# Kernel tuning notes

Hardware: AMD Instinct MI355X
Metric: run time of the kernel (lower is better)

## Reference

```python
import jax, jax.numpy as jnp
import numpy as np

TEMPERATURE = 0.1
THRESHOLD = 0.2
EPS = 1e-12


def setup_inputs() -> dict:
    key = jax.random.key(0)
    k0, k1 = jax.random.split(key)
    f0 = jax.random.normal(k0, (1, 256, 80, 80), dtype=jnp.float32)
    f1 = jax.random.normal(k1, (1, 256, 80, 80), dtype=jnp.float32)
    return {"f0": f0, "f1": f1}


def reference(f0, f1):
    B, C, H0, W0 = f0.shape
    _, _, H1, W1 = f1.shape
    N0, N1 = H0 * W0, H1 * W1

    # (B, N, C), L2-normalized along C (matches F.normalize with eps clamp)
    f0_flat = f0.reshape(B, C, N0).transpose(0, 2, 1)
    f1_flat = f1.reshape(B, C, N1).transpose(0, 2, 1)
    f0n = f0_flat / jnp.maximum(jnp.linalg.norm(f0_flat, axis=-1, keepdims=True), EPS)
    f1n = f1_flat / jnp.maximum(jnp.linalg.norm(f1_flat, axis=-1, keepdims=True), EPS)

    # cosine similarity / temperature: (B, N0, N1)
    S = jnp.einsum('bnc,bmc->bnm', f0n, f1n) / TEMPERATURE
    # dual softmax
    P = jax.nn.softmax(S, axis=-1) * jax.nn.softmax(S, axis=-2)

    # mutual nearest-neighbor matching (B == 1 branch)
    conf = jnp.max(P[0], axis=-1)              # (N0,)
    indices0 = jnp.argmax(P[0], axis=-1)       # (N0,) row argmax
    indices1 = jnp.argmax(P[0], axis=-2)       # (N1,) column argmax
    ar0 = jnp.arange(N0)
    mutual = indices1[indices0] == ar0
    valid = mutual & (conf > THRESHOLD)        # (N0,) bool

    # fixed-shape (jit-friendly) match outputs: full grid, zeroed where invalid
    mkpts0 = jnp.stack([ar0 % W0, ar0 // W0], axis=1).astype(jnp.float32)
    mkpts1 = jnp.stack([indices0 % W1, indices0 // W1], axis=1).astype(jnp.float32)
    vf = valid[:, None].astype(jnp.float32)
    mkpts0 = mkpts0 * vf
    mkpts1 = mkpts1 * vf
    mconf = jnp.where(valid, conf, 0.0)

    return (P, mkpts0, mkpts1, mconf, valid)
```

## Files before the change

kernel.cpp:

```cpp
#include <hip/hip_runtime.h>

#define N0 6400
#define NC 256
#define WW 80

using half8   = __attribute__((ext_vector_type(8))) _Float16;
using floatx4 = __attribute__((ext_vector_type(4))) float;
#define GLOBAL_AS __attribute__((address_space(1)))
#define LDS_AS    __attribute__((address_space(3)))

__device__ __forceinline__ unsigned long long packvi(float v, int i) {
    return ((unsigned long long)__float_as_uint(v) << 32) | (unsigned int)i;
}

__global__ __launch_bounds__(256) void knorm(const float* __restrict__ f0,
                                             const float* __restrict__ f1,
                                             float* __restrict__ inv0,
                                             float* __restrict__ inv1) {
    int t = blockIdx.x * 256 + threadIdx.x;
    const float* src = (t < N0) ? f0 : f1;
    int n = (t < N0) ? t : (t - N0);
    float s = 0.f;
#pragma unroll 8
    for (int c = 0; c < NC; ++c) {
        float v = src[c * N0 + n];
        s += v * v;
    }
    float inv = 1.0f / fmaxf(sqrtf(s), 1e-12f);
    if (t < N0) inv0[n] = inv; else inv1[n] = inv;
}

__global__ __launch_bounds__(256) void ktrans(const float* __restrict__ f0,
                                              const float* __restrict__ f1,
                                              const float* __restrict__ inv0,
                                              const float* __restrict__ inv1,
                                              _Float16* __restrict__ A2,
                                              _Float16* __restrict__ B2) {
    __shared__ float tile[32][33];
    const float* src = blockIdx.z ? f1 : f0;
    const float* inv = blockIdx.z ? inv1 : inv0;
    _Float16* dst    = blockIdx.z ? B2 : A2;
    int t = threadIdx.x;
    int n0 = blockIdx.x * 32, c0 = blockIdx.y * 32;
    int tx = t & 31, ty = t >> 5;
#pragma unroll
    for (int u = 0; u < 4; ++u)
        tile[ty + u * 8][tx] = src[(c0 + ty + u * 8) * N0 + n0 + tx];
    __syncthreads();
    int row = t >> 3;
    int cg  = (t & 7) * 4;
    int n = n0 + row;
    float iv = inv[n];
    union { ushort4 u4; _Float16 h[4]; } pk;
#pragma unroll
    for (int u = 0; u < 4; ++u)
        pk.h[u] = (_Float16)(tile[cg + u][row] * iv);
    *(ushort4*)&dst[n * NC + c0 + cg] = pk.u4;
}

__device__ __forceinline__ void stage_panel(const _Float16* __restrict__ G,
                                            unsigned short* lds, int r0, int tid) {
    int rl = tid >> 3;
    int ch = ((tid & 7) ^ (rl & 7)) * 8;
#pragma unroll
    for (int kk = 0; kk < 4; ++kk)
#pragma unroll
        for (int g = 0; g < 4; ++g) {
            const _Float16* ga = G + (r0 + g * 32 + rl) * NC + kk * 64 + ch;
            __builtin_amdgcn_global_load_lds((const GLOBAL_AS unsigned int*)ga,
                (LDS_AS unsigned int*)&lds[kk * 8192 + g * 2048 + tid * 8], 16, 0, 0);
        }
}

__device__ __forceinline__ void tile_mfma(const unsigned short* ldsA,
                                          const unsigned short* ldsB,
                                          int lane, int wm, int wn,
                                          floatx4 acc[4][4]) {
    int q = lane >> 4;
#pragma unroll
    for (int s = 0; s < 8; ++s) {
        int c  = s * 4 + q;
        int kk = c >> 3, cq = c & 7;
        half8 af[4], bf[4];
#pragma unroll
        for (int mt = 0; mt < 4; ++mt) {
            int ra = wm * 64 + mt * 16 + (lane & 15);
            af[mt] = *(const half8*)&ldsA[kk * 8192 + ra * 64 + ((cq ^ (ra & 7)) * 8)];
            int rb = wn * 64 + mt * 16 + (lane & 15);
            bf[mt] = *(const half8*)&ldsB[kk * 8192 + rb * 64 + ((cq ^ (rb & 7)) * 8)];
        }
#pragma unroll
        for (int mt = 0; mt < 4; ++mt)
#pragma unroll
            for (int nt = 0; nt < 4; ++nt)
                acc[mt][nt] = __builtin_amdgcn_mfma_f32_16x16x32_f16(
                    af[mt], bf[nt], acc[mt][nt], 0, 0, 0);
    }
}

__global__ __launch_bounds__(256, 1) void kgemm1(const _Float16* __restrict__ A2,
                                                 const _Float16* __restrict__ B2,
                                                 float* __restrict__ rowsum,
                                                 float* __restrict__ colsum) {
    __shared__ __align__(16) unsigned short ldsA[32768], ldsB[32768];
    int tid = threadIdx.x, lane = tid & 63, wave = tid >> 6;
    int wm = wave & 1, wn = wave >> 1, q = lane >> 4;
    int i0 = blockIdx.x * 128, jp = blockIdx.y * 1280;

    stage_panel(A2, ldsA, i0, tid);
    float rsum[4][4] = {};

    for (int jt = 0; jt < 10; ++jt) {
        __syncthreads();
        stage_panel(B2, ldsB, jp + jt * 128, tid);
        __syncthreads();
        floatx4 acc[4][4] = {};
        tile_mfma(ldsA, ldsB, lane, wm, wn, acc);

        float csum[4] = {0.f, 0.f, 0.f, 0.f};
#pragma unroll
        for (int mt = 0; mt < 4; ++mt)
#pragma unroll
            for (int r = 0; r < 4; ++r) {
                float rv = 0.f;
#pragma unroll
                for (int nt = 0; nt < 4; ++nt) {
                    float e = __expf(10.0f * acc[mt][nt][r]);
                    rv += e; csum[nt] += e;
                }
                rsum[mt][r] += rv;
            }
#pragma unroll
        for (int nt = 0; nt < 4; ++nt) {
            csum[nt] += __shfl_xor(csum[nt], 16);
            csum[nt] += __shfl_xor(csum[nt], 32);
        }
        if (lane < 16)
#pragma unroll
            for (int nt = 0; nt < 4; ++nt)
                atomicAdd(&colsum[jp + jt * 128 + wn * 64 + nt * 16 + lane], csum[nt]);
    }
#pragma unroll
    for (int mt = 0; mt < 4; ++mt)
#pragma unroll
        for (int r = 0; r < 4; ++r) {
            float v = rsum[mt][r];
            v += __shfl_xor(v, 1);
            v += __shfl_xor(v, 2);
            v += __shfl_xor(v, 4);
            v += __shfl_xor(v, 8);
            if ((lane & 15) == 0)
                atomicAdd(&rowsum[i0 + wm * 64 + mt * 16 + q * 4 + r], v);
        }
}

__global__ __launch_bounds__(256, 1) void kgemm2(const _Float16* __restrict__ A2,
                                                 const _Float16* __restrict__ B2,
                                                 const float* __restrict__ rowsum,
                                                 const float* __restrict__ colsum,
                                                 float* __restrict__ P,
                                                 unsigned long long* __restrict__ rowbest,
                                                 unsigned long long* __restrict__ colbest) {
    __shared__ __align__(16) unsigned short ldsA[32768], ldsB[32768];
    int tid = threadIdx.x, lane = tid & 63, wave = tid >> 6;
    int wm = wave & 1, wn = wave >> 1, q = lane >> 4;
    int i0 = blockIdx.x * 128, jp = blockIdx.y * 1280;

    stage_panel(A2, ldsA, i0, tid);

    float ir[4][4];
#pragma unroll
    for (int mt = 0; mt < 4; ++mt) {
        float4 v4 = *(const float4*)&rowsum[i0 + wm * 64 + mt * 16 + q * 4];
        ir[mt][0] = 1.0f / v4.x; ir[mt][1] = 1.0f / v4.y;
        ir[mt][2] = 1.0f / v4.z; ir[mt][3] = 1.0f / v4.w;
    }

    unsigned long long rbv[4][4] = {};

    for (int jt = 0; jt < 10; ++jt) {
        __syncthreads();
        stage_panel(B2, ldsB, jp + jt * 128, tid);
        __syncthreads();
        floatx4 acc[4][4] = {};
        tile_mfma(ldsA, ldsB, lane, wm, wn, acc);

        int cb0 = jp + jt * 128 + wn * 64 + (lane & 15);
        float ic[4];
#pragma unroll
        for (int nt = 0; nt < 4; ++nt) ic[nt] = 1.0f / colsum[cb0 + nt * 16];

        unsigned long long colb[4] = {0ull, 0ull, 0ull, 0ull};
#pragma unroll
        for (int mt = 0; mt < 4; ++mt) {
            int rb0 = i0 + wm * 64 + mt * 16 + q * 4;
#pragma unroll
            for (int r = 0; r < 4; ++r) {
                int row = rb0 + r;
#pragma unroll
                for (int nt = 0; nt < 4; ++nt) {
                    float pv = __expf(20.0f * acc[mt][nt][r]) * ir[mt][r] * ic[nt];
                    P[row * N0 + cb0 + nt * 16] = pv;
                    unsigned long long pr = packvi(pv, cb0 + nt * 16);
                    if (pr > rbv[mt][r]) rbv[mt][r] = pr;
                    unsigned long long pc = packvi(pv, row);
                    if (pc > colb[nt]) colb[nt] = pc;
                }
            }
        }
#pragma unroll
        for (int nt = 0; nt < 4; ++nt) {
            unsigned long long o = __shfl_xor(colb[nt], 16);
            if (o > colb[nt]) colb[nt] = o;
            o = __shfl_xor(colb[nt], 32);
            if (o > colb[nt]) colb[nt] = o;
        }
        if (lane < 16)
#pragma unroll
            for (int nt = 0; nt < 4; ++nt)
                atomicMax(&colbest[cb0 + nt * 16], colb[nt]);
    }
#pragma unroll
    for (int mt = 0; mt < 4; ++mt)
#pragma unroll
        for (int r = 0; r < 4; ++r) {
            unsigned long long v = rbv[mt][r];
#pragma unroll
            for (int s = 1; s < 16; s <<= 1) {
                unsigned long long o = __shfl_xor(v, s);
                if (o > v) v = o;
            }
            if ((lane & 15) == 0)
                atomicMax(&rowbest[i0 + wm * 64 + mt * 16 + q * 4 + r], v);
        }
}

__global__ __launch_bounds__(256) void kmatch(const unsigned long long* __restrict__ rowbest,
                                              const unsigned long long* __restrict__ colbest,
                                              float* __restrict__ out) {
    int i = blockIdx.x * 256 + threadIdx.x;
    unsigned long long rb = rowbest[i];
    float conf = __uint_as_float((unsigned int)(rb >> 32));
    int jj = (int)(rb & 0xffffffffu);
    unsigned long long cb = colbest[jj];
    int i2 = (int)(cb & 0xffffffffu);
    bool valid = (i2 == i) && (conf > 0.2f);
    float vf = valid ? 1.0f : 0.0f;

    float* mk0   = out + 40960000;
    float* mk1   = out + 40972800;
    float* mconf = out + 40985600;
    float* vout  = out + 40992000;
    mk0[i * 2 + 0] = vf * (float)(i % WW);
    mk0[i * 2 + 1] = vf * (float)(i / WW);
    mk1[i * 2 + 0] = vf * (float)(jj % WW);
    mk1[i * 2 + 1] = vf * (float)(jj / WW);
    mconf[i] = valid ? conf : 0.0f;
    vout[i]  = vf;
}

extern "C" void kernel_launch(void* const* d_in, const int* in_sizes, int n_in,
                              void* d_out, int out_size, void* d_ws, size_t ws_size,
                              hipStream_t stream) {
    const float* f0 = (const float*)d_in[0];
    const float* f1 = (const float*)d_in[1];
    float* out = (float*)d_out;

    _Float16* A2 = (_Float16*)d_ws;
    _Float16* B2 = A2 + 6400 * 256;
    float* inv0   = (float*)(B2 + 6400 * 256);
    float* inv1   = inv0 + 6400;
    float* rowsum = inv1 + 6400;
    float* colsum = rowsum + 6400;
    unsigned long long* rowbest = (unsigned long long*)(colsum + 6400);
    unsigned long long* colbest = rowbest + 6400;

    hipMemsetAsync(rowsum, 0, 153600, stream);

    knorm<<<50, 256, 0, stream>>>(f0, f1, inv0, inv1);
    ktrans<<<dim3(200, 8, 2), 256, 0, stream>>>(f0, f1, inv0, inv1, A2, B2);
    kgemm1<<<dim3(50, 5), 256, 0, stream>>>(A2, B2, rowsum, colsum);
    kgemm2<<<dim3(50, 5), 256, 0, stream>>>(A2, B2, rowsum, colsum,
                                            out, rowbest, colbest);
    kmatch<<<25, 256, 0, stream>>>(rowbest, colbest, out);
}
```

Baseline: 275.1 us.

## Keep A fragments in registers and double-buffer B panels in LDS

Both GEMM kernels now load the A panel fragments into registers once, then reuse the whole 128KB LDS as two B-panel buffers. The next B panel is prefetched with global_load_lds while MFMAs run on the current one, leaving one barrier per iteration instead of two. The memset is also folded into knorm to remove a separate launch. The cost is heavy register pressure (128 VGPRs for A fragments plus accumulators), and the async LDS loads rely on the end-of-iteration barrier to be complete before the buffer is read.

Result: faster. 267.9 us (-2.6%).

```diff
diff --git a/kernel.cpp b/kernel.cpp
--- a/kernel.cpp
+++ b/kernel.cpp
@@ -16,8 +16,16 @@
 __global__ __launch_bounds__(256) void knorm(const float* __restrict__ f0,
                                              const float* __restrict__ f1,
                                              float* __restrict__ inv0,
-                                             float* __restrict__ inv1) {
+                                             float* __restrict__ inv1,
+                                             float* __restrict__ rowsum,
+                                             float* __restrict__ colsum,
+                                             unsigned long long* __restrict__ rowbest,
+                                             unsigned long long* __restrict__ colbest) {
     int t = blockIdx.x * 256 + threadIdx.x;
+    if (t < N0) {
+        rowsum[t] = 0.f; colsum[t] = 0.f;
+        rowbest[t] = 0ull; colbest[t] = 0ull;
+    }
     const float* src = (t < N0) ? f0 : f1;
     int n = (t < N0) ? t : (t - N0);
     float s = 0.f;
@@ -72,50 +80,54 @@
         }
 }
 
-__device__ __forceinline__ void tile_mfma(const unsigned short* ldsA,
-                                          const unsigned short* ldsB,
-                                          int lane, int wm, int wn,
-                                          floatx4 acc[4][4]) {
-    int q = lane >> 4;
-#pragma unroll
-    for (int s = 0; s < 8; ++s) {
-        int c  = s * 4 + q;
-        int kk = c >> 3, cq = c & 7;
-        half8 af[4], bf[4];
-#pragma unroll
-        for (int mt = 0; mt < 4; ++mt) {
-            int ra = wm * 64 + mt * 16 + (lane & 15);
-            af[mt] = *(const half8*)&ldsA[kk * 8192 + ra * 64 + ((cq ^ (ra & 7)) * 8)];
-            int rb = wn * 64 + mt * 16 + (lane & 15);
-            bf[mt] = *(const half8*)&ldsB[kk * 8192 + rb * 64 + ((cq ^ (rb & 7)) * 8)];
-        }
-#pragma unroll
-        for (int mt = 0; mt < 4; ++mt)
-#pragma unroll
-            for (int nt = 0; nt < 4; ++nt)
-                acc[mt][nt] = __builtin_amdgcn_mfma_f32_16x16x32_f16(
-                    af[mt], bf[nt], acc[mt][nt], 0, 0, 0);
-    }
-}
-
 __global__ __launch_bounds__(256, 1) void kgemm1(const _Float16* __restrict__ A2,
                                                  const _Float16* __restrict__ B2,
                                                  float* __restrict__ rowsum,
                                                  float* __restrict__ colsum) {
-    __shared__ __align__(16) unsigned short ldsA[32768], ldsB[32768];
+    __shared__ __align__(16) unsigned short lds[65536];
     int tid = threadIdx.x, lane = tid & 63, wave = tid >> 6;
     int wm = wave & 1, wn = wave >> 1, q = lane >> 4;
     int i0 = blockIdx.x * 128, jp = blockIdx.y * 1280;
 
-    stage_panel(A2, ldsA, i0, tid);
+    stage_panel(A2, lds, i0, tid);
+    stage_panel(B2, lds + 32768, jp, tid);
+    __syncthreads();
+
+    half8 af[4][8];
+#pragma unroll
+    for (int mt = 0; mt < 4; ++mt)
+#pragma unroll
+        for (int s = 0; s < 8; ++s) {
+            int c = s * 4 + q, kk = c >> 3, cq = c & 7;
+            int ra = wm * 64 + mt * 16 + (lane & 15);
+            af[mt][s] = *(const half8*)&lds[kk * 8192 + ra * 64 + ((cq ^ (ra & 7)) * 8)];
+        }
+    __syncthreads();
+
     float rsum[4][4] = {};
 
     for (int jt = 0; jt < 10; ++jt) {
-        __syncthreads();
-        stage_panel(B2, ldsB, jp + jt * 128, tid);
-        __syncthreads();
+        const unsigned short* cur = lds + ((jt & 1) ? 0 : 32768);
+        if (jt < 9)
+            stage_panel(B2, lds + ((jt & 1) ? 32768 : 0), jp + (jt + 1) * 128, tid);
+
         floatx4 acc[4][4] = {};
-        tile_mfma(ldsA, ldsB, lane, wm, wn, acc);
+#pragma unroll
+        for (int s = 0; s < 8; ++s) {
+            int c = s * 4 + q, kk = c >> 3, cq = c & 7;
+            half8 bf[4];
+#pragma unroll
+            for (int nt = 0; nt < 4; ++nt) {
+                int rb = wn * 64 + nt * 16 + (lane & 15);
+                bf[nt] = *(const half8*)&cur[kk * 8192 + rb * 64 + ((cq ^ (rb & 7)) * 8)];
+            }
+#pragma unroll
+            for (int mt = 0; mt < 4; ++mt)
+#pragma unroll
+                for (int nt = 0; nt < 4; ++nt)
+                    acc[mt][nt] = __builtin_amdgcn_mfma_f32_16x16x32_f16(
+                        af[mt][s], bf[nt], acc[mt][nt], 0, 0, 0);
+        }
 
         float csum[4] = {0.f, 0.f, 0.f, 0.f};
 #pragma unroll
@@ -139,6 +151,7 @@
 #pragma unroll
             for (int nt = 0; nt < 4; ++nt)
                 atomicAdd(&colsum[jp + jt * 128 + wn * 64 + nt * 16 + lane], csum[nt]);
+        __syncthreads();
     }
 #pragma unroll
     for (int mt = 0; mt < 4; ++mt)
@@ -161,12 +174,25 @@
                                                  float* __restrict__ P,
                                                  unsigned long long* __restrict__ rowbest,
                                                  unsigned long long* __restrict__ colbest) {
-    __shared__ __align__(16) unsigned short ldsA[32768], ldsB[32768];
+    __shared__ __align__(16) unsigned short lds[65536];
     int tid = threadIdx.x, lane = tid & 63, wave = tid >> 6;
     int wm = wave & 1, wn = wave >> 1, q = lane >> 4;
     int i0 = blockIdx.x * 128, jp = blockIdx.y * 1280;
 
-    stage_panel(A2, ldsA, i0, tid);
+    stage_panel(A2, lds, i0, tid);
+    stage_panel(B2, lds + 32768, jp, tid);
+    __syncthreads();
+
+    half8 af[4][8];
+#pragma unroll
+    for (int mt = 0; mt < 4; ++mt)
+#pragma unroll
+        for (int s = 0; s < 8; ++s) {
+            int c = s * 4 + q, kk = c >> 3, cq = c & 7;
+            int ra = wm * 64 + mt * 16 + (lane & 15);
+            af[mt][s] = *(const half8*)&lds[kk * 8192 + ra * 64 + ((cq ^ (ra & 7)) * 8)];
+        }
+    __syncthreads();
 
     float ir[4][4];
 #pragma unroll
@@ -179,11 +205,27 @@
     unsigned long long rbv[4][4] = {};
 
     for (int jt = 0; jt < 10; ++jt) {
-        __syncthreads();
-        stage_panel(B2, ldsB, jp + jt * 128, tid);
-        __syncthreads();
+        const unsigned short* cur = lds + ((jt & 1) ? 0 : 32768);
+        if (jt < 9)
+            stage_panel(B2, lds + ((jt & 1) ? 32768 : 0), jp + (jt + 1) * 128, tid);
+
         floatx4 acc[4][4] = {};
-        tile_mfma(ldsA, ldsB, lane, wm, wn, acc);
+#pragma unroll
+        for (int s = 0; s < 8; ++s) {
+            int c = s * 4 + q, kk = c >> 3, cq = c & 7;
+            half8 bf[4];
+#pragma unroll
+            for (int nt = 0; nt < 4; ++nt) {
+                int rb = wn * 64 + nt * 16 + (lane & 15);
+                bf[nt] = *(const half8*)&cur[kk * 8192 + rb * 64 + ((cq ^ (rb & 7)) * 8)];
+            }
+#pragma unroll
+            for (int mt = 0; mt < 4; ++mt)
+#pragma unroll
+                for (int nt = 0; nt < 4; ++nt)
+                    acc[mt][nt] = __builtin_amdgcn_mfma_f32_16x16x32_f16(
+                        af[mt][s], bf[nt], acc[mt][nt], 0, 0, 0);
+        }
 
         int cb0 = jp + jt * 128 + wn * 64 + (lane & 15);
         float ic[4];
@@ -219,6 +261,7 @@
 #pragma unroll
             for (int nt = 0; nt < 4; ++nt)
                 atomicMax(&colbest[cb0 + nt * 16], colb[nt]);
+        __syncthreads();
     }
 #pragma unroll
     for (int mt = 0; mt < 4; ++mt)
@@ -275,9 +318,8 @@
     unsigned long long* rowbest = (unsigned long long*)(colsum + 6400);
     unsigned long long* colbest = rowbest + 6400;
 
-    hipMemsetAsync(rowsum, 0, 153600, stream);
-
-    knorm<<<50, 256, 0, stream>>>(f0, f1, inv0, inv1);
+    knorm<<<50, 256, 0, stream>>>(f0, f1, inv0, inv1,
+                                  rowsum, colsum, rowbest, colbest);
     ktrans<<<dim3(200, 8, 2), 256, 0, stream>>>(f0, f1, inv0, inv1, A2, B2);
     kgemm1<<<dim3(50, 5), 256, 0, stream>>>(A2, B2, rowsum, colsum);
     kgemm2<<<dim3(50, 5), 256, 0, stream>>>(A2, B2, rowsum, colsum,
```

## Halve GEMM LDS footprint, keep A low-K in registers, double grid, fuse memset

Applied to the files above, without the earlier changes.

The GEMM kernels drop from 128KB to 64KB of LDS. The low half of the A panel's K dimension now lives in registers and the B panel is staged in two K-chunks, so two blocks can fit per CU. The column split is doubled to 10 so the grid grows from 250 to 500 blocks, which gives better CU coverage. The norm kernel is split across two channel halves for more parallelism, and it now zeroes the accumulators in place of the separate memset. The cost is extra barriers per tile, higher register pressure from holding the A fragments, and twice as many atomic updates.

Measured after the change: 280.9 us. +2.1%, slower.

```diff
diff --git a/kernel.cpp b/kernel.cpp
--- a/kernel.cpp
+++ b/kernel.cpp
@@ -15,30 +15,37 @@
 
 __global__ __launch_bounds__(256) void knorm(const float* __restrict__ f0,
                                              const float* __restrict__ f1,
-                                             float* __restrict__ inv0,
-                                             float* __restrict__ inv1) {
-    int t = blockIdx.x * 256 + threadIdx.x;
-    const float* src = (t < N0) ? f0 : f1;
-    int n = (t < N0) ? t : (t - N0);
+                                             float* __restrict__ snorm,
+                                             float* __restrict__ rowsum,
+                                             float* __restrict__ colsum,
+                                             unsigned long long* __restrict__ rowbest,
+                                             unsigned long long* __restrict__ colbest) {
+    int g = blockIdx.x * 256 + threadIdx.x;
+    if (g < N0) {
+        rowsum[g] = 0.f; colsum[g] = 0.f;
+        rowbest[g] = 0ull; colbest[g] = 0ull;
+    }
+    int h = (g >= 12800) ? 1 : 0;
+    int j = g - h * 12800;
+    const float* src = (j < N0) ? f0 : f1;
+    int n = (j < N0) ? j : (j - N0);
+    int c0 = h * 128;
     float s = 0.f;
 #pragma unroll 8
-    for (int c = 0; c < NC; ++c) {
-        float v = src[c * N0 + n];
+    for (int c = 0; c < 128; ++c) {
+        float v = src[(c0 + c) * N0 + n];
         s += v * v;
     }
-    float inv = 1.0f / fmaxf(sqrtf(s), 1e-12f);
-    if (t < N0) inv0[n] = inv; else inv1[n] = inv;
+    snorm[g] = s;
 }
 
 __global__ __launch_bounds__(256) void ktrans(const float* __restrict__ f0,
                                               const float* __restrict__ f1,
-                                              const float* __restrict__ inv0,
-                                              const float* __restrict__ inv1,
+                                              const float* __restrict__ snorm,
                                               _Float16* __restrict__ A2,
                                               _Float16* __restrict__ B2) {
     __shared__ float tile[32][33];
     const float* src = blockIdx.z ? f1 : f0;
-    const float* inv = blockIdx.z ? inv1 : inv0;
     _Float16* dst    = blockIdx.z ? B2 : A2;
     int t = threadIdx.x;
     int n0 = blockIdx.x * 32, c0 = blockIdx.y * 32;
@@ -50,7 +57,9 @@
     int row = t >> 3;
     int cg  = (t & 7) * 4;
     int n = n0 + row;
-    float iv = inv[n];
+    int j = (blockIdx.z ? N0 : 0) + n;
+    float s = snorm[j] + snorm[12800 + j];
+    float iv = 1.0f / fmaxf(sqrtf(s), 1e-12f);
     union { ushort4 u4; _Float16 h[4]; } pk;
 #pragma unroll
     for (int u = 0; u < 4; ++u)
@@ -58,36 +67,45 @@
     *(ushort4*)&dst[n * NC + c0 + cg] = pk.u4;
 }
 
-__device__ __forceinline__ void stage_panel(const _Float16* __restrict__ G,
-                                            unsigned short* lds, int r0, int tid) {
+__device__ __forceinline__ void stage_chunk(const _Float16* __restrict__ G,
+                                            unsigned short* lds, int r0, int kc,
+                                            int tid) {
     int rl = tid >> 3;
     int ch = ((tid & 7) ^ (rl & 7)) * 8;
 #pragma unroll
-    for (int kk = 0; kk < 4; ++kk)
+    for (int kk = 0; kk < 2; ++kk)
 #pragma unroll
         for (int g = 0; g < 4; ++g) {
-            const _Float16* ga = G + (r0 + g * 32 + rl) * NC + kk * 64 + ch;
+            const _Float16* ga = G + (r0 + g * 32 + rl) * NC + kc * 128 + kk * 64 + ch;
             __builtin_amdgcn_global_load_lds((const GLOBAL_AS unsigned int*)ga,
                 (LDS_AS unsigned int*)&lds[kk * 8192 + g * 2048 + tid * 8], 16, 0, 0);
         }
 }
 
-__device__ __forceinline__ void tile_mfma(const unsigned short* ldsA,
-                                          const unsigned short* ldsB,
-                                          int lane, int wm, int wn,
-                                          floatx4 acc[4][4]) {
+template<bool HI>
+__device__ __forceinline__ void compute_half(const unsigned short* bbuf,
+                                             const unsigned short* abufHi,
+                                             const half8 aflo[4][4],
+                                             int lane, int wm, int wn,
+                                             floatx4 acc[4][4]) {
     int q = lane >> 4;
 #pragma unroll
-    for (int s = 0; s < 8; ++s) {
-        int c  = s * 4 + q;
-        int kk = c >> 3, cq = c & 7;
+    for (int s = 0; s < 4; ++s) {
+        int c = s * 4 + q, kk = c >> 3, cq = c & 7;
         half8 af[4], bf[4];
 #pragma unroll
         for (int mt = 0; mt < 4; ++mt) {
-            int ra = wm * 64 + mt * 16 + (lane & 15);
-            af[mt] = *(const half8*)&ldsA[kk * 8192 + ra * 64 + ((cq ^ (ra & 7)) * 8)];
             int rb = wn * 64 + mt * 16 + (lane & 15);
-            bf[mt] = *(const half8*)&ldsB[kk * 8192 + rb * 64 + ((cq ^ (rb & 7)) * 8)];
+            bf[mt] = *(const half8*)&bbuf[kk * 8192 + rb * 64 + ((cq ^ (rb & 7)) * 8)];
+        }
+#pragma unroll
+        for (int mt = 0; mt < 4; ++mt) {
+            if (HI) {
+                int ra = wm * 64 + mt * 16 + (lane & 15);
+                af[mt] = *(const half8*)&abufHi[kk * 8192 + ra * 64 + ((cq ^ (ra & 7)) * 8)];
+            } else {
+                af[mt] = aflo[mt][s];
+            }
         }
 #pragma unroll
         for (int mt = 0; mt < 4; ++mt)
@@ -98,24 +116,42 @@
     }
 }
 
-__global__ __launch_bounds__(256, 1) void kgemm1(const _Float16* __restrict__ A2,
+__global__ __launch_bounds__(256, 2) void kgemm1(const _Float16* __restrict__ A2,
                                                  const _Float16* __restrict__ B2,
                                                  float* __restrict__ rowsum,
                                                  float* __restrict__ colsum) {
-    __shared__ __align__(16) unsigned short ldsA[32768], ldsB[32768];
+    __shared__ __align__(16) unsigned short lds[32768];
+    unsigned short* regA = lds;
+    unsigned short* regB = lds + 16384;
     int tid = threadIdx.x, lane = tid & 63, wave = tid >> 6;
     int wm = wave & 1, wn = wave >> 1, q = lane >> 4;
-    int i0 = blockIdx.x * 128, jp = blockIdx.y * 1280;
-
-    stage_panel(A2, ldsA, i0, tid);
+    int i0 = blockIdx.x * 128, jp = blockIdx.y * 640;
+
+    stage_chunk(A2, regB, i0, 0, tid);
+    stage_chunk(A2, regA, i0, 1, tid);
+    __syncthreads();
+    half8 aflo[4][4];
+#pragma unroll
+    for (int mt = 0; mt < 4; ++mt)
+#pragma unroll
+        for (int s = 0; s < 4; ++s) {
+            int c = s * 4 + q, kk = c >> 3, cq = c & 7;
+            int ra = wm * 64 + mt * 16 + (lane & 15);
+            aflo[mt][s] = *(const half8*)&regB[kk * 8192 + ra * 64 + ((cq ^ (ra & 7)) * 8)];
+        }
+    __syncthreads();
+
     float rsum[4][4] = {};
 
-    for (int jt = 0; jt < 10; ++jt) {
-        __syncthreads();
-        stage_panel(B2, ldsB, jp + jt * 128, tid);
+    for (int jt = 0; jt < 5; ++jt) {
+        stage_chunk(B2, regB, jp + jt * 128, 0, tid);
         __syncthreads();
         floatx4 acc[4][4] = {};
-        tile_mfma(ldsA, ldsB, lane, wm, wn, acc);
+        compute_half<false>(regB, regA, aflo, lane, wm, wn, acc);
+        __syncthreads();
+        stage_chunk(B2, regB, jp + jt * 128, 1, tid);
+        __syncthreads();
+        compute_half<true>(regB, regA, aflo, lane, wm, wn, acc);
 
         float csum[4] = {0.f, 0.f, 0.f, 0.f};
 #pragma unroll
@@ -139,6 +175,7 @@
 #pragma unroll
             for (int nt = 0; nt < 4; ++nt)
                 atomicAdd(&colsum[jp + jt * 128 + wn * 64 + nt * 16 + lane], csum[nt]);
+        __syncthreads();
     }
 #pragma unroll
     for (int mt = 0; mt < 4; ++mt)
@@ -154,19 +191,33 @@
         }
 }
 
-__global__ __launch_bounds__(256, 1) void kgemm2(const _Float16* __restrict__ A2,
+__global__ __launch_bounds__(256, 2) void kgemm2(const _Float16* __restrict__ A2,
                                                  const _Float16* __restrict__ B2,
                                                  const float* __restrict__ rowsum,
                                                  const float* __restrict__ colsum,
                                                  float* __restrict__ P,
                                                  unsigned long long* __restrict__ rowbest,
                                                  unsigned long long* __restrict__ colbest) {
-    __shared__ __align__(16) unsigned short ldsA[32768], ldsB[32768];
+    __shared__ __align__(16) unsigned short lds[32768];
+    unsigned short* regA = lds;
+    unsigned short* regB = lds + 16384;
     int tid = threadIdx.x, lane = tid & 63, wave = tid >> 6;
     int wm = wave & 1, wn = wave >> 1, q = lane >> 4;
-    int i0 = blockIdx.x * 128, jp = blockIdx.y * 1280;
-
-    stage_panel(A2, ldsA, i0, tid);
+    int i0 = blockIdx.x * 128, jp = blockIdx.y * 640;
+
+    stage_chunk(A2, regB, i0, 0, tid);
+    stage_chunk(A2, regA, i0, 1, tid);
+    __syncthreads();
+    half8 aflo[4][4];
+#pragma unroll
+    for (int mt = 0; mt < 4; ++mt)
+#pragma unroll
+        for (int s = 0; s < 4; ++s) {
+            int c = s * 4 + q, kk = c >> 3, cq = c & 7;
+            int ra = wm * 64 + mt * 16 + (lane & 15);
+            aflo[mt][s] = *(const half8*)&regB[kk * 8192 + ra * 64 + ((cq ^ (ra & 7)) * 8)];
+        }
+    __syncthreads();
 
     float ir[4][4];
 #pragma unroll
@@ -178,12 +229,15 @@
 
     unsigned long long rbv[4][4] = {};
 
-    for (int jt = 0; jt < 10; ++jt) {
-        __syncthreads();
-        stage_panel(B2, ldsB, jp + jt * 128, tid);
+    for (int jt = 0; jt < 5; ++jt) {
+        stage_chunk(B2, regB, jp + jt * 128, 0, tid);
         __syncthreads();
         floatx4 acc[4][4] = {};
-        tile_mfma(ldsA, ldsB, lane, wm, wn, acc);
+        compute_half<false>(regB, regA, aflo, lane, wm, wn, acc);
+        __syncthreads();
+        stage_chunk(B2, regB, jp + jt * 128, 1, tid);
+        __syncthreads();
+        compute_half<true>(regB, regA, aflo, lane, wm, wn, acc);
 
         int cb0 = jp + jt * 128 + wn * 64 + (lane & 15);
         float ic[4];
@@ -219,6 +273,7 @@
 #pragma unroll
             for (int nt = 0; nt < 4; ++nt)
                 atomicMax(&colbest[cb0 + nt * 16], colb[nt]);
+        __syncthreads();
     }
 #pragma unroll
     for (int mt = 0; mt < 4; ++mt)
@@ -268,19 +323,17 @@
 
     _Float16* A2 = (_Float16*)d_ws;
     _Float16* B2 = A2 + 6400 * 256;
-    float* inv0   = (float*)(B2 + 6400 * 256);
-    float* inv1   = inv0 + 6400;
-    float* rowsum = inv1 + 6400;
+    float* snorm  = (float*)(B2 + 6400 * 256);
+    float* rowsum = snorm + 25600;
     float* colsum = rowsum + 6400;
     unsigned long long* rowbest = (unsigned long long*)(colsum + 6400);
     unsigned long long* colbest = rowbest + 6400;
 
-    hipMemsetAsync(rowsum, 0, 153600, stream);
-
-    knorm<<<50, 256, 0, stream>>>(f0, f1, inv0, inv1);
-    ktrans<<<dim3(200, 8, 2), 256, 0, stream>>>(f0, f1, inv0, inv1, A2, B2);
-    kgemm1<<<dim3(50, 5), 256, 0, stream>>>(A2, B2, rowsum, colsum);
-    kgemm2<<<dim3(50, 5), 256, 0, stream>>>(A2, B2, rowsum, colsum,
-                                            out, rowbest, colbest);
+    knorm<<<100, 256, 0, stream>>>(f0, f1, snorm,
+                                   rowsum, colsum, rowbest, colbest);
+    ktrans<<<dim3(200, 8, 2), 256, 0, stream>>>(f0, f1, snorm, A2, B2);
+    kgemm1<<<dim3(50, 10), 256, 0, stream>>>(A2, B2, rowsum, colsum);
+    kgemm2<<<dim3(50, 10), 256, 0, stream>>>(A2, B2, rowsum, colsum,
+                                             out, rowbest, colbest);
     kmatch<<<25, 256, 0, stream>>>(rowbest, colbest, out);
 }
```
